# Performance work log

Measured on AMD Instinct MI355X. Metric: run time of the kernel, lower is better.

## Reference

```python
import jax, jax.numpy as jnp
import numpy as np

NEG_INF = -9e9  # matches torch code's -9000000000.0


def setup_inputs() -> dict:
    key = jax.random.key(0)
    ks = jax.random.split(key, 12)
    B, N, L = 128, 32, 36
    Ds, Dv, H = 512, 1024, 512
    span_embeddings = jax.random.normal(ks[0], (B, N, Ds), dtype=jnp.float32)
    image_embeddings = jax.random.normal(ks[1], (B, L, Dv), dtype=jnp.float32)
    span_mask = jax.random.randint(ks[2], (B, N), 0, 2).astype(jnp.float32)
    image_mask = jax.random.randint(ks[3], (B, L), 0, 2).astype(jnp.float32)
    # BilinearPairWiseClassifier weight: maps span dim -> image dim
    Wg = jax.random.normal(ks[4], (Ds, Dv), dtype=jnp.float32) / np.sqrt(Ds)
    # SimplePairWiseClassifier MLP on concat(first, second, first*second)
    W1 = jax.random.normal(ks[5], (3 * Ds, H), dtype=jnp.float32) / np.sqrt(3 * Ds)
    b1 = jnp.zeros((H,), dtype=jnp.float32)
    W2 = jax.random.normal(ks[6], (H, H), dtype=jnp.float32) / np.sqrt(H)
    b2 = jnp.zeros((H,), dtype=jnp.float32)
    W3 = jax.random.normal(ks[7], (H, 1), dtype=jnp.float32) / np.sqrt(H)
    b3 = jnp.zeros((1,), dtype=jnp.float32)
    return {
        "span_embeddings": span_embeddings,
        "image_embeddings": image_embeddings,
        "span_mask": span_mask,
        "image_mask": image_mask,
        "Wg": Wg, "W1": W1, "b1": b1, "W2": W2, "b2": b2, "W3": W3, "b3": b3,
    }


def reference(span_embeddings, image_embeddings, span_mask, image_mask,
              Wg, W1, b1, W2, b2, W3, b3):
    B, N, Ds = span_embeddings.shape
    L = image_embeddings.shape[1]

    # ---- score_grounding (vectorized B^2 loop) ----
    # mention_scores[b] = bilinear(first[b], second[b]); the off-diagonal
    # 'score' in the original loop recomputes the SAME thing (only the mask
    # varies with jdx), so one (B,N,L) tensor suffices.
    M = jnp.einsum('bnd,de,ble->bnl', span_embeddings, Wg, image_embeddings)  # (B,N,L)
    # pairwise mask over doc pairs (i uses span_mask, j uses image_mask)
    pm = span_mask[:, None, :, None] * image_mask[None, :, None, :]  # (B,B,N,L)
    pm = jnp.where(pm != 0, pm, NEG_INF)
    w = jax.nn.softmax(pm.reshape(B, B, N * L), axis=-1).reshape(B, B, N, L)
    sent_scores = jnp.einsum('inl,ijnl->ij', M, w)  # (B,B)

    # ---- score_text: all span pairs via combinations(range(N), 2) ----
    iu, ju = np.triu_indices(N, k=1)  # same order as itertools.combinations
    first = span_embeddings[:, iu]    # (B,P,Ds)
    second = span_embeddings[:, ju]   # (B,P,Ds)
    feat = jnp.concatenate([first, second, first * second], axis=-1)  # (B,P,3Ds)
    h = jax.nn.relu(feat @ W1 + b1)
    h = jax.nn.relu(h @ W2 + b2)
    text_scores = (h @ W3 + b3)[..., 0]  # (B,P)

    # ---- contrastive loss over sentence-score matrix ----
    loss = (-jnp.sum(jax.nn.log_softmax(sent_scores, axis=1))
            - jnp.sum(jax.nn.log_softmax(sent_scores.T, axis=1))) / B
    return loss, M, text_scores
```

## Files before the change

### kernel.cpp

```cpp
#include <hip/hip_runtime.h>

#define B_  128
#define N_  32
#define L_  36
#define DS  512
#define DV  1024
#define H_  512
#define P_  496
#define R_  63488
#define LSE_BLKS 128

typedef __attribute__((ext_vector_type(8))) short bf16x8;
typedef __attribute__((ext_vector_type(4))) float f32x4;

__device__ __forceinline__ ushort f2bf(float x){
  unsigned u = __builtin_bit_cast(unsigned, x);
  return (ushort)((u + 0x7FFFu + ((u >> 16) & 1u)) >> 16);
}
__device__ __forceinline__ float bf2f(ushort u){
  unsigned v = ((unsigned)u) << 16;
  return __builtin_bit_cast(float, v);
}

__device__ __forceinline__ bf16x8 pkmul(bf16x8 a, bf16x8 b){
  bf16x8 o;
  #pragma unroll
  for (int e = 0; e < 8; ++e)
    o[e] = (short)f2bf(bf2f((ushort)a[e]) * bf2f((ushort)b[e]));
  return o;
}

__device__ __forceinline__ void gload16(const void* g, void* l){
  __builtin_amdgcn_global_load_lds((const __attribute__((address_space(1))) unsigned*)g,
                                   (__attribute__((address_space(3))) unsigned*)l, 16, 0, 0);
}

__device__ __forceinline__ float wave_sum(float v){
  #pragma unroll
  for (int m = 32; m >= 1; m >>= 1) v += __shfl_xor(v, m);
  return v;
}
__device__ __forceinline__ float wave_max(float v){
  #pragma unroll
  for (int m = 32; m >= 1; m >>= 1) v = fmaxf(v, __shfl_xor(v, m));
  return v;
}

#define SPAN_F4 524288
#define IMG_F4  1179648
#define CONV_BLKS ((SPAN_F4 + IMG_F4) / 256)
#define TR_BLKS   (512 * 5)
__global__ void prep_all(const float* __restrict__ span, const float* __restrict__ img,
                         const float* __restrict__ b3,
                         const float* __restrict__ Wg, const float* __restrict__ W1,
                         const float* __restrict__ W2,
                         const float* __restrict__ sm, const float* __restrict__ im,
                         ushort* __restrict__ spbf, ushort* __restrict__ imgbf,
                         float* __restrict__ text,
                         ushort* __restrict__ WgT, ushort* __restrict__ UVBT,
                         ushort* __restrict__ W1cT, ushort* __restrict__ W2T,
                         float* cnt_s, float* cnt_i, int* iu, int* ju, float* loss){
  __shared__ float tile[32][33];
  const int bid = blockIdx.x, tid = threadIdx.x;
  if (bid < CONV_BLKS){
    int idx = bid * 256 + tid;
    if (idx < R_) text[idx] = b3[0];
    const float* src; ushort* dst; int k;
    if (idx < SPAN_F4){ src = span; dst = spbf; k = idx; }
    else              { src = img;  dst = imgbf; k = idx - SPAN_F4; }
    float4 v = *(const float4*)&src[(size_t)k * 4];
    ushort4 o; o.x = f2bf(v.x); o.y = f2bf(v.y); o.z = f2bf(v.z); o.w = f2bf(v.w);
    *(ushort4*)&dst[(size_t)k * 4] = o;
  } else if (bid < CONV_BLKS + TR_BLKS){
    int b = bid - CONV_BLKS;
    int z = b >> 9, rem = b & 511;
    int bx = rem & 31, by = rem >> 5;
    const float* src; ushort* dst; int Nn;
    if      (z == 0){ src = Wg;            dst = WgT;            Nn = 1024; }
    else if (z == 1){ src = W1;            dst = UVBT;           Nn = 512;  }
    else if (z == 2){ src = W1 + 512*512;  dst = UVBT + 512*512; Nn = 512;  }
    else if (z == 3){ src = W1 + 1024*512; dst = W1cT;           Nn = 512;  }
    else            { src = W2;            dst = W2T;            Nn = 512;  }
    if (bx * 32 >= Nn) return;
    int n0 = bx * 32, k0 = by * 32;
    int x = tid & 31, y = tid >> 5;
    #pragma unroll
    for (int i = 0; i < 4; ++i) tile[y + 8*i][x] = src[(k0 + y + 8*i) * Nn + n0 + x];
    __syncthreads();
    #pragma unroll
    for (int i = 0; i < 4; ++i) dst[(n0 + y + 8*i) * 512 + k0 + x] = f2bf(tile[x][y + 8*i]);
  } else {
    int t = (bid - CONV_BLKS - TR_BLKS) * 256 + tid;
    if (t < P_){
      int i = 0, rem = t, cnt = N_ - 1;
      while (rem >= cnt){ rem -= cnt; ++i; --cnt; }
      iu[t] = i; ju[t] = i + 1 + rem;
    }
    if (t < B_){
      float s = 0.f;
      for (int n = 0; n < N_; ++n) s += sm[t*N_ + n];
      cnt_s[t] = s;
    } else if (t < 2*B_){
      int j = t - B_;
      float s = 0.f;
      for (int l = 0; l < L_; ++l) s += im[j*L_ + l];
      cnt_i[j] = s;
    }
    if (t == 0) loss[0] = 0.f;
  }
}

__device__ __forceinline__ void mfma_phase(const ushort* cA, const ushort* cB,
                                           int wm, int wn, int fm, int quad,
                                           f32x4 acc[4][4]){
  bf16x8 af[4], bg[4];
  #pragma unroll
  for (int i = 0; i < 4; ++i){
    af[i] = *(const bf16x8*)&cA[(wm + i * 16 + fm) * 32 + quad * 8];
    bg[i] = *(const bf16x8*)&cB[(wn + i * 16 + fm) * 32 + quad * 8];
  }
  asm volatile("s_waitcnt lgkmcnt(0)" ::: "memory");
  __builtin_amdgcn_s_barrier();
  #pragma unroll
  for (int i = 0; i < 4; ++i)
    #pragma unroll
    for (int j = 0; j < 4; ++j)
      acc[i][j] = __builtin_amdgcn_mfma_f32_16x16x32_bf16(af[i], bg[j], acc[i][j], 0, 0, 0);
}

__device__ __forceinline__ void mma_mainloop(const ushort* __restrict__ A,
                                             const ushort* __restrict__ BT,
                                             size_t m0, int n0,
                                             ushort* sA0, ushort* sA1,
                                             ushort* sB0, ushort* sB1,
                                             f32x4 acc[4][4]){
  const int tid = threadIdx.x, wid = tid >> 6, lane = tid & 63;
  const int wm = (wid >> 1) * 64, wn = (wid & 1) * 64;
  const int quad = lane >> 4, fm = lane & 15;
  const char* gA = (const char*)A + (m0 + (size_t)(wid * 32 + (lane >> 2))) * 1024 + (lane & 3) * 16;
  const char* gB = (const char*)BT + ((size_t)n0 + wid * 32 + (lane >> 2)) * 1024 + (lane & 3) * 16;
  const int wb = wid * 1024;

  #define STG_ML(dA, dB, ks)                                   \
    do {                                                       \
      gload16(gA + (ks) * 64,             (dA) + wb);          \
      gload16(gA + (ks) * 64 + 16 * 1024, (dA) + wb + 512);    \
      gload16(gB + (ks) * 64,             (dB) + wb);          \
      gload16(gB + (ks) * 64 + 16 * 1024, (dB) + wb + 512);    \
    } while (0)

  STG_ML(sA0, sB0, 0);
  #pragma unroll
  for (int ks = 0; ks < 16; ks += 2){
    STG_ML(sA1, sB1, ks + 1);
    asm volatile("s_waitcnt vmcnt(4)" ::: "memory");
    __builtin_amdgcn_s_barrier();
    mfma_phase(sA0, sB0, wm, wn, fm, quad, acc);
    if (ks + 2 < 16){
      STG_ML(sA0, sB0, ks + 2);
      asm volatile("s_waitcnt vmcnt(4)" ::: "memory");
    } else {
      asm volatile("s_waitcnt vmcnt(0)" ::: "memory");
    }
    __builtin_amdgcn_s_barrier();
    mfma_phase(sA1, sB1, wm, wn, fm, quad, acc);
  }
  #undef STG_ML
}

__global__ __launch_bounds__(256, 4) void span2_makez(const ushort* __restrict__ A,
                                                      const ushort* __restrict__ BT2,
                                                      ushort* __restrict__ SG,
                                                      ushort* __restrict__ UV,
                                                      const int* __restrict__ iu,
                                                      const int* __restrict__ ju,
                                                      ushort* __restrict__ Z){
  __shared__ ushort sA0[4096], sA1[4096], sB0[4096], sB1[4096];
  if (blockIdx.x < 512){
    f32x4 acc[4][4] = {};
    size_t m0 = (size_t)(blockIdx.x >> 4) * 128;
    int ng = (blockIdx.x & 15) * 128;
    mma_mainloop(A, BT2, m0, ng, sA0, sA1, sB0, sB1, acc);
    const int tid = threadIdx.x, wid = tid >> 6, lane = tid & 63;
    const int wm = (wid >> 1) * 64, wn = (wid & 1) * 64, quad = lane >> 4, fm = lane & 15;
    ushort* C = (ng < 1024) ? SG : UV;
    const int nbase = (ng < 1024) ? ng : (ng - 1024);
    #pragma unroll
    for (int i = 0; i < 4; ++i)
      #pragma unroll
      for (int r = 0; r < 4; ++r){
        size_t row = m0 + wm + i * 16 + quad * 4 + r;
        #pragma unroll
        for (int j = 0; j < 4; ++j){
          int col = nbase + wn + j * 16 + fm;
          C[row * 1024 + col] = f2bf(acc[i][j][r]);
        }
      }
  } else {
    int idx = (blockIdx.x - 512) * 256 + threadIdx.x;
    int r = idx >> 6, k = (idx & 63) << 3;
    int b = r / P_, p = r - b * P_;
    bf16x8 x = *(const bf16x8*)&A[(size_t)(b * N_ + iu[p]) * 512 + k];
    bf16x8 y = *(const bf16x8*)&A[(size_t)(b * N_ + ju[p]) * 512 + k];
    *(bf16x8*)&Z[(size_t)r * 512 + k] = pkmul(x, y);
  }
}

__global__ __launch_bounds__(256) void batched_m_mfma(const ushort* __restrict__ SGbf,
                                                      const ushort* __restrict__ imgbf,
                                                      const float* __restrict__ sm,
                                                      float* __restrict__ Mout,
                                                      float* __restrict__ Msum,
                                                      float* __restrict__ Mtot){
  const int b = blockIdx.x;
  const int tid = threadIdx.x, wid = tid >> 6, lane = tid & 63;
  const int quad = lane >> 4, fm = lane & 15;
  __shared__ float red[4][32][48];
  __shared__ float shr[4];
  f32x4 acc[2][3] = {};
  const int wk = wid * 256;
  const ushort* Ab = SGbf + (size_t)b * 32 * 1024;
  const ushort* Bb = imgbf + (size_t)b * 36 * 1024;
  #pragma unroll
  for (int ks = 0; ks < 8; ++ks){
    const int k = wk + ks * 32 + quad * 8;
    bf16x8 af[2], bg[3];
    af[0] = *(const bf16x8*)&Ab[(0*16 + fm) * 1024 + k];
    af[1] = *(const bf16x8*)&Ab[(1*16 + fm) * 1024 + k];
    bg[0] = *(const bf16x8*)&Bb[(0*16 + fm) * 1024 + k];
    bg[1] = *(const bf16x8*)&Bb[(1*16 + fm) * 1024 + k];
    bg[2] = *(const bf16x8*)&Bb[(2*16 + fm) * 1024 + k];
    #pragma unroll
    for (int i = 0; i < 2; ++i)
      #pragma unroll
      for (int j = 0; j < 3; ++j)
        acc[i][j] = __builtin_amdgcn_mfma_f32_16x16x32_bf16(af[i], bg[j], acc[i][j], 0, 0, 0);
  }
  #pragma unroll
  for (int i = 0; i < 2; ++i)
    #pragma unroll
    for (int j = 0; j < 3; ++j)
      #pragma unroll
      for (int r = 0; r < 4; ++r)
        red[wid][i*16 + quad*4 + r][j*16 + fm] = acc[i][j][r];
  __syncthreads();
  float tot = 0.f;
  #pragma unroll
  for (int q = 0; q < 5; ++q){
    int out = tid + 256 * q;
    if (out < N_*L_){
      int n = out / L_, l = out - n * L_;
      float v = red[0][n][l] + red[1][n][l] + red[2][n][l] + red[3][n][l];
      Mout[b * (N_*L_) + out] = v;
      tot += v;
    }
  }
  tot = wave_sum(tot);
  if (lane == 0) shr[wid] = tot;
  __syncthreads();
  if (tid == 0) Mtot[b] = shr[0] + shr[1] + shr[2] + shr[3];
  if (tid < L_){
    float s = 0.f;
    for (int n = 0; n < N_; ++n){
      float mv = red[0][n][tid] + red[1][n][tid] + red[2][n][tid] + red[3][n][tid];
      s += mv * sm[b*N_ + n];
    }
    Msum[b*L_ + tid] = s;
  }
}

__device__ void lse_loss_body(const float* __restrict__ Msum, const float* __restrict__ im,
                              const float* __restrict__ cnt_s, const float* __restrict__ cnt_i,
                              const float* __restrict__ Mtot, float* __restrict__ out,
                              int i, float* sh ){
  const int tid = threadIdx.x;
  const int t = tid & 127;
  const int w4 = tid >> 6, lane = tid & 63;
  float sr = 0.f, sc = 0.f;
  #pragma unroll 4
  for (int l = 0; l < L_; ++l){
    sr += Msum[i*L_ + l] * im[t*L_ + l];
    sc += Msum[t*L_ + l] * im[i*L_ + l];
  }
  const float dr = cnt_s[i] * cnt_i[t];
  const float vr = (dr != 0.f) ? (sr / dr) : (Mtot[i] * (1.f/(float)(N_*L_)));
  const float dc = cnt_s[t] * cnt_i[i];
  const float vc = (dc != 0.f) ? (sc / dc) : (Mtot[t] * (1.f/(float)(N_*L_)));

  float m = wave_max(vr);
  if (lane == 0) sh[w4] = m;
  __syncthreads();
  const float mr = fmaxf(sh[0], sh[1]);
  __syncthreads();
  float e = wave_sum(expf(vr - mr));
  if (lane == 0) sh[w4] = e;
  __syncthreads();
  const float ser = sh[0] + sh[1];
  __syncthreads();
  float rs = wave_sum(vr);
  if (lane == 0) sh[w4] = rs;
  __syncthreads();
  const float rst = sh[0] + sh[1];
  __syncthreads();
  float mc0 = wave_max(vc);
  if (lane == 0) sh[w4] = mc0;
  __syncthreads();
  const float mc = fmaxf(sh[0], sh[1]);
  __syncthreads();
  float ec = wave_sum(expf(vc - mc));
  if (lane == 0) sh[w4] = ec;
  __syncthreads();
  const float sec = sh[0] + sh[1];
  if (tid == 0){
    float contrib = (mr + logf(ser)) + (mc + logf(sec)) - 2.f * rst / (float)B_;
    atomicAdd(out, contrib);
  }
}

__device__ __forceinline__ void mma_loop_k64(const ushort* __restrict__ A,
                                             const ushort* __restrict__ BT,
                                             size_t m0, int n0,
                                             ushort* sA0, ushort* sA1,
                                             ushort* sB0, ushort* sB1,
                                             f32x4 acc[4][4]){
  const int tid = threadIdx.x, wid = tid >> 6, lane = tid & 63;
  const int wm = (wid >> 1) * 64, wn = (wid & 1) * 64;
  const int quad = lane >> 4, fm = lane & 15;
  const int r64 = tid >> 2, ch = (tid & 3) * 8;
  const ushort* gA = A + (m0 + r64) * 512 + ch;
  const ushort* gB = BT + (size_t)(n0 + r64) * 512 + ch;

  #define STG_K(dA, dB, ks)                                   \
    do {                                                      \
      const int k0_ = (ks) * 32;                              \
      gload16(gA + k0_,            (dA) + tid * 8);           \
      gload16(gA + 64*512 + k0_,   (dA) + 2048 + tid * 8);    \
      gload16(gB + k0_,            (dB) + tid * 8);           \
      gload16(gB + 64*512 + k0_,   (dB) + 2048 + tid * 8);    \
    } while (0)

  STG_K(sA0, sB0, 0);
  #pragma unroll
  for (int ks = 0; ks < 16; ks += 2){
    STG_K(sA1, sB1, ks + 1);
    asm volatile("s_waitcnt vmcnt(4)" ::: "memory");
    __builtin_amdgcn_s_barrier();
    mfma_phase(sA0, sB0, wm, wn, fm, quad, acc);
    if (ks + 2 < 16){
      STG_K(sA0, sB0, ks + 2);
      asm volatile("s_waitcnt vmcnt(4)" ::: "memory");
    } else {
      asm volatile("s_waitcnt vmcnt(0)" ::: "memory");
    }
    __builtin_amdgcn_s_barrier();
    mfma_phase(sA1, sB1, wm, wn, fm, quad, acc);
  }
  #undef STG_K
}

__device__ __forceinline__ void tile_map(int bid, int& m0, int& n0){
  int x = bid & 7;
  int q = bid >> 3;
  int m = x * 62 + (q >> 2);
  m0 = m * 128;
  n0 = (q & 3) * 128;
}

__global__ __launch_bounds__(256, 4) void gemm_z(const ushort* __restrict__ Z,
                                                 const ushort* __restrict__ W1cT,
                                                 const ushort* __restrict__ UV,
                                                 const float* __restrict__ b1,
                                                 const int* __restrict__ iu,
                                                 const int* __restrict__ ju,
                                                 ushort* __restrict__ h1){
  __shared__ ushort sA0[4096], sA1[4096], sB0[4096], sB1[4096];
  f32x4 acc[4][4] = {};
  int m0i, n0; tile_map(blockIdx.x, m0i, n0);
  const size_t m0 = (size_t)m0i;
  mma_loop_k64(Z, W1cT, m0, n0, sA0, sA1, sB0, sB1, acc);
  const int tid = threadIdx.x, wid = tid >> 6, lane = tid & 63;
  const int wm = (wid >> 1) * 64, wn = (wid & 1) * 64, quad = lane >> 4, fm = lane & 15;
  #pragma unroll
  for (int i = 0; i < 4; ++i)
    #pragma unroll
    for (int r = 0; r < 4; ++r){
      int row = (int)m0 + wm + i * 16 + quad * 4 + r;
      int b = row / P_, p = row - b * P_;
      const ushort* Ur = UV + (size_t)(b * N_ + iu[p]) * 1024;
      const ushort* Vr = UV + (size_t)(b * N_ + ju[p]) * 1024 + 512;
      #pragma unroll
      for (int j = 0; j < 4; ++j){
        int col = n0 + wn + j * 16 + fm;
        float h = acc[i][j][r] + bf2f(Ur[col]) + bf2f(Vr[col]) + b1[col];
        h1[(size_t)row * 512 + col] = f2bf(fmaxf(h, 0.f));
      }
    }
}

__global__ __launch_bounds__(256, 4) void gemm_h2(const ushort* __restrict__ h1,
                                                  const ushort* __restrict__ W2T,
                                                  const float* __restrict__ b2,
                                                  const float* __restrict__ W3,
                                                  float* __restrict__ text,
                                                  const float* __restrict__ Msum,
                                                  const float* __restrict__ im,
                                                  const float* __restrict__ cnt_s,
                                                  const float* __restrict__ cnt_i,
                                                  const float* __restrict__ Mtot,
                                                  float* __restrict__ loss){
  __shared__ ushort smem[16384];
  if (blockIdx.x < LSE_BLKS){
    lse_loss_body(Msum, im, cnt_s, cnt_i, Mtot, loss, blockIdx.x, (float*)smem);
    return;
  }
  ushort* sA0 = smem;
  ushort* sA1 = smem + 4096;
  ushort* sB0 = smem + 8192;
  ushort* sB1 = smem + 12288;
  f32x4 acc[4][4] = {};
  int m0i, n0; tile_map(blockIdx.x - LSE_BLKS, m0i, n0);
  const size_t m0 = (size_t)m0i;
  mma_loop_k64(h1, W2T, m0, n0, sA0, sA1, sB0, sB1, acc);
  const int tid = threadIdx.x, wid = tid >> 6, lane = tid & 63;
  const int wm = (wid >> 1) * 64, wn = (wid & 1) * 64, quad = lane >> 4, fm = lane & 15;
  float w3v[4], b2v[4];
  #pragma unroll
  for (int j = 0; j < 4; ++j){
    int col = n0 + wn + j * 16 + fm;
    w3v[j] = W3[col]; b2v[j] = b2[col];
  }
  #pragma unroll
  for (int i = 0; i < 4; ++i)
    #pragma unroll
    for (int r = 0; r < 4; ++r){
      int row = (int)m0 + wm + i * 16 + quad * 4 + r;
      float s = 0.f;
      #pragma unroll
      for (int j = 0; j < 4; ++j){
        float h = fmaxf(acc[i][j][r] + b2v[j], 0.f);
        s = fmaf(h, w3v[j], s);
      }
      s += __shfl_xor(s, 1); s += __shfl_xor(s, 2); s += __shfl_xor(s, 4); s += __shfl_xor(s, 8);
      if (fm == 0) atomicAdd(&text[row], s);
    }
}

extern "C" void kernel_launch(void* const* d_in, const int* in_sizes, int n_in,
                              void* d_out, int out_size, void* d_ws, size_t ws_size,
                              hipStream_t stream) {
  const float* span = (const float*)d_in[0];
  const float* img  = (const float*)d_in[1];
  const float* sm   = (const float*)d_in[2];
  const float* im   = (const float*)d_in[3];
  const float* Wg   = (const float*)d_in[4];
  const float* W1   = (const float*)d_in[5];
  const float* b1   = (const float*)d_in[6];
  const float* W2   = (const float*)d_in[7];
  const float* b2   = (const float*)d_in[8];
  const float* W3   = (const float*)d_in[9];
  const float* b3   = (const float*)d_in[10];

  float* out  = (float*)d_out;
  float* loss = out;
  float* Mout = out + 1;
  float* text = out + 1 + B_*N_*L_;

  ushort* wsu  = (ushort*)d_ws;
  ushort* Zbf  = wsu;
  ushort* h1bf = Zbf + (size_t)R_*512;
  ushort* UVbf = h1bf + (size_t)R_*512;
  ushort* SGbf = UVbf + (size_t)4096*1024;
  ushort* spbf = SGbf + (size_t)4096*1024;
  ushort* imgbf= spbf + 4096*512;
  ushort* BT2  = imgbf + (size_t)(B_*L_ + 12)*1024;
  ushort* WgT  = BT2;
  ushort* UVBT = BT2 + 1024*512;
  ushort* W1cT = UVBT + 1024*512;
  ushort* W2T  = W1cT + 512*512;
  float* Msum  = (float*)(W2T + 512*512);
  float* Mtot  = Msum + B_*L_;
  float* cnt_s = Mtot + B_;
  float* cnt_i = cnt_s + B_;
  int*   iu    = (int*)(cnt_i + B_);
  int*   ju    = iu + P_;

  prep_all<<<CONV_BLKS + TR_BLKS + 2, 256, 0, stream>>>(
      span, img, b3, Wg, W1, W2, sm, im,
      spbf, imgbf, text, WgT, UVBT, W1cT, W2T, cnt_s, cnt_i, iu, ju, loss);

  span2_makez<<<512 + R_*512/8/256, 256, 0, stream>>>(spbf, BT2, SGbf, UVbf, iu, ju, Zbf);

  batched_m_mfma<<<B_, 256, 0, stream>>>(SGbf, imgbf, sm, Mout, Msum, Mtot);

  gemm_z<<<1984, 256, 0, stream>>>(Zbf, W1cT, UVbf, b1, iu, ju, h1bf);
  gemm_h2<<<LSE_BLKS + 1984, 256, 0, stream>>>(
      h1bf, W2T, b2, W3, text, Msum, im, cnt_s, cnt_i, Mtot, loss);
}
```

Before: 237.1 us.

## Triple-buffer LDS staging in GEMM mainloops with MFMA priority boost

```diff
diff --git a/kernel.cpp b/kernel.cpp
--- a/kernel.cpp
+++ b/kernel.cpp
@@ -110,29 +110,30 @@
   }
 }
 
-__device__ __forceinline__ void mfma_phase(const ushort* cA, const ushort* cB,
-                                           int wm, int wn, int fm, int quad,
-                                           f32x4 acc[4][4]){
-  bf16x8 af[4], bg[4];
+__device__ __forceinline__ void frag_ld(const ushort* cA, const ushort* cB,
+                                        int wm, int wn, int fm, int quad,
+                                        bf16x8 af[4], bf16x8 bg[4]){
   #pragma unroll
   for (int i = 0; i < 4; ++i){
     af[i] = *(const bf16x8*)&cA[(wm + i * 16 + fm) * 32 + quad * 8];
     bg[i] = *(const bf16x8*)&cB[(wn + i * 16 + fm) * 32 + quad * 8];
   }
-  asm volatile("s_waitcnt lgkmcnt(0)" ::: "memory");
-  __builtin_amdgcn_s_barrier();
+}
+__device__ __forceinline__ void mfma16(const bf16x8 af[4], const bf16x8 bg[4], f32x4 acc[4][4]){
+  __builtin_amdgcn_s_setprio(1);
   #pragma unroll
   for (int i = 0; i < 4; ++i)
     #pragma unroll
     for (int j = 0; j < 4; ++j)
       acc[i][j] = __builtin_amdgcn_mfma_f32_16x16x32_bf16(af[i], bg[j], acc[i][j], 0, 0, 0);
+  __builtin_amdgcn_s_setprio(0);
 }
 
 __device__ __forceinline__ void mma_mainloop(const ushort* __restrict__ A,
                                              const ushort* __restrict__ BT,
                                              size_t m0, int n0,
-                                             ushort* sA0, ushort* sA1,
-                                             ushort* sB0, ushort* sB1,
+                                             ushort* sA0, ushort* sA1, ushort* sA2,
+                                             ushort* sB0, ushort* sB1, ushort* sB2,
                                              f32x4 acc[4][4]){
   const int tid = threadIdx.x, wid = tid >> 6, lane = tid & 63;
   const int wm = (wid >> 1) * 64, wn = (wid & 1) * 64;
@@ -140,47 +141,48 @@
   const char* gA = (const char*)A + (m0 + (size_t)(wid * 32 + (lane >> 2))) * 1024 + (lane & 3) * 16;
   const char* gB = (const char*)BT + ((size_t)n0 + wid * 32 + (lane >> 2)) * 1024 + (lane & 3) * 16;
   const int wb = wid * 1024;
-
-  #define STG_ML(dA, dB, ks)                                   \
-    do {                                                       \
-      gload16(gA + (ks) * 64,             (dA) + wb);          \
-      gload16(gA + (ks) * 64 + 16 * 1024, (dA) + wb + 512);    \
-      gload16(gB + (ks) * 64,             (dB) + wb);          \
-      gload16(gB + (ks) * 64 + 16 * 1024, (dB) + wb + 512);    \
+  ushort* const bA[3] = {sA0, sA1, sA2};
+  ushort* const bB[3] = {sB0, sB1, sB2};
+
+  #define STG_ML(bi, ks)                                           \
+    do {                                                           \
+      gload16(gA + (ks) * 64,             bA[bi] + wb);            \
+      gload16(gA + (ks) * 64 + 16 * 1024, bA[bi] + wb + 512);      \
+      gload16(gB + (ks) * 64,             bB[bi] + wb);            \
+      gload16(gB + (ks) * 64 + 16 * 1024, bB[bi] + wb + 512);      \
     } while (0)
 
-  STG_ML(sA0, sB0, 0);
-  #pragma unroll
-  for (int ks = 0; ks < 16; ks += 2){
-    STG_ML(sA1, sB1, ks + 1);
-    asm volatile("s_waitcnt vmcnt(4)" ::: "memory");
+  STG_ML(0, 0); STG_ML(1, 1); STG_ML(2, 2);
+  #pragma unroll
+  for (int ks = 0; ks < 16; ++ks){
+    if (ks < 14)       asm volatile("s_waitcnt vmcnt(8)" ::: "memory");
+    else if (ks == 14) asm volatile("s_waitcnt vmcnt(4)" ::: "memory");
+    else               asm volatile("s_waitcnt vmcnt(0)" ::: "memory");
     __builtin_amdgcn_s_barrier();
-    mfma_phase(sA0, sB0, wm, wn, fm, quad, acc);
-    if (ks + 2 < 16){
-      STG_ML(sA0, sB0, ks + 2);
-      asm volatile("s_waitcnt vmcnt(4)" ::: "memory");
-    } else {
-      asm volatile("s_waitcnt vmcnt(0)" ::: "memory");
-    }
+    bf16x8 af[4], bg[4];
+    frag_ld(bA[ks % 3], bB[ks % 3], wm, wn, fm, quad, af, bg);
+    asm volatile("s_waitcnt lgkmcnt(0)" ::: "memory");
+    __builtin_amdgcn_sched_barrier(0);
     __builtin_amdgcn_s_barrier();
-    mfma_phase(sA1, sB1, wm, wn, fm, quad, acc);
+    if (ks + 3 < 16) STG_ML(ks % 3, ks + 3);
+    mfma16(af, bg, acc);
   }
   #undef STG_ML
 }
 
-__global__ __launch_bounds__(256, 4) void span2_makez(const ushort* __restrict__ A,
+__global__ __launch_bounds__(256, 3) void span2_makez(const ushort* __restrict__ A,
                                                       const ushort* __restrict__ BT2,
                                                       ushort* __restrict__ SG,
                                                       ushort* __restrict__ UV,
                                                       const int* __restrict__ iu,
                                                       const int* __restrict__ ju,
                                                       ushort* __restrict__ Z){
-  __shared__ ushort sA0[4096], sA1[4096], sB0[4096], sB1[4096];
+  __shared__ ushort sA0[4096], sA1[4096], sA2[4096], sB0[4096], sB1[4096], sB2[4096];
   if (blockIdx.x < 512){
     f32x4 acc[4][4] = {};
     size_t m0 = (size_t)(blockIdx.x >> 4) * 128;
     int ng = (blockIdx.x & 15) * 128;
-    mma_mainloop(A, BT2, m0, ng, sA0, sA1, sB0, sB1, acc);
+    mma_mainloop(A, BT2, m0, ng, sA0, sA1, sA2, sB0, sB1, sB2, acc);
     const int tid = threadIdx.x, wid = tid >> 6, lane = tid & 63;
     const int wm = (wid >> 1) * 64, wn = (wid & 1) * 64, quad = lane >> 4, fm = lane & 15;
     ushort* C = (ng < 1024) ? SG : UV;
@@ -320,8 +322,8 @@
 __device__ __forceinline__ void mma_loop_k64(const ushort* __restrict__ A,
                                              const ushort* __restrict__ BT,
                                              size_t m0, int n0,
-                                             ushort* sA0, ushort* sA1,
-                                             ushort* sB0, ushort* sB1,
+                                             ushort* sA0, ushort* sA1, ushort* sA2,
+                                             ushort* sB0, ushort* sB1, ushort* sB2,
                                              f32x4 acc[4][4]){
   const int tid = threadIdx.x, wid = tid >> 6, lane = tid & 63;
   const int wm = (wid >> 1) * 64, wn = (wid & 1) * 64;
@@ -329,31 +331,32 @@
   const int r64 = tid >> 2, ch = (tid & 3) * 8;
   const ushort* gA = A + (m0 + r64) * 512 + ch;
   const ushort* gB = BT + (size_t)(n0 + r64) * 512 + ch;
-
-  #define STG_K(dA, dB, ks)                                   \
-    do {                                                      \
-      const int k0_ = (ks) * 32;                              \
-      gload16(gA + k0_,            (dA) + tid * 8);           \
-      gload16(gA + 64*512 + k0_,   (dA) + 2048 + tid * 8);    \
-      gload16(gB + k0_,            (dB) + tid * 8);           \
-      gload16(gB + 64*512 + k0_,   (dB) + 2048 + tid * 8);    \
+  ushort* const bA[3] = {sA0, sA1, sA2};
+  ushort* const bB[3] = {sB0, sB1, sB2};
+
+  #define STG_K(bi, ks)                                        \
+    do {                                                       \
+      const int k0_ = (ks) * 32;                               \
+      gload16(gA + k0_,            bA[bi] + tid * 8);          \
+      gload16(gA + 64*512 + k0_,   bA[bi] + 2048 + tid * 8);   \
+      gload16(gB + k0_,            bB[bi] + tid * 8);          \
+      gload16(gB + 64*512 + k0_,   bB[bi] + 2048 + tid * 8);   \
     } while (0)
 
-  STG_K(sA0, sB0, 0);
-  #pragma unroll
-  for (int ks = 0; ks < 16; ks += 2){
-    STG_K(sA1, sB1, ks + 1);
-    asm volatile("s_waitcnt vmcnt(4)" ::: "memory");
+  STG_K(0, 0); STG_K(1, 1); STG_K(2, 2);
+  #pragma unroll
+  for (int ks = 0; ks < 16; ++ks){
+    if (ks < 14)       asm volatile("s_waitcnt vmcnt(8)" ::: "memory");
+    else if (ks == 14) asm volatile("s_waitcnt vmcnt(4)" ::: "memory");
+    else               asm volatile("s_waitcnt vmcnt(0)" ::: "memory");
     __builtin_amdgcn_s_barrier();
-    mfma_phase(sA0, sB0, wm, wn, fm, quad, acc);
-    if (ks + 2 < 16){
-      STG_K(sA0, sB0, ks + 2);
-      asm volatile("s_waitcnt vmcnt(4)" ::: "memory");
-    } else {
-      asm volatile("s_waitcnt vmcnt(0)" ::: "memory");
-    }
+    bf16x8 af[4], bg[4];
+    frag_ld(bA[ks % 3], bB[ks % 3], wm, wn, fm, quad, af, bg);
+    asm volatile("s_waitcnt lgkmcnt(0)" ::: "memory");
+    __builtin_amdgcn_sched_barrier(0);
     __builtin_amdgcn_s_barrier();
-    mfma_phase(sA1, sB1, wm, wn, fm, quad, acc);
+    if (ks + 3 < 16) STG_K(ks % 3, ks + 3);
+    mfma16(af, bg, acc);
   }
   #undef STG_K
 }
@@ -366,18 +369,18 @@
   n0 = (q & 3) * 128;
 }
 
-__global__ __launch_bounds__(256, 4) void gemm_z(const ushort* __restrict__ Z,
+__global__ __launch_bounds__(256, 3) void gemm_z(const ushort* __restrict__ Z,
                                                  const ushort* __restrict__ W1cT,
                                                  const ushort* __restrict__ UV,
                                                  const float* __restrict__ b1,
                                                  const int* __restrict__ iu,
                                                  const int* __restrict__ ju,
                                                  ushort* __restrict__ h1){
-  __shared__ ushort sA0[4096], sA1[4096], sB0[4096], sB1[4096];
+  __shared__ ushort sA0[4096], sA1[4096], sA2[4096], sB0[4096], sB1[4096], sB2[4096];
   f32x4 acc[4][4] = {};
   int m0i, n0; tile_map(blockIdx.x, m0i, n0);
   const size_t m0 = (size_t)m0i;
-  mma_loop_k64(Z, W1cT, m0, n0, sA0, sA1, sB0, sB1, acc);
+  mma_loop_k64(Z, W1cT, m0, n0, sA0, sA1, sA2, sB0, sB1, sB2, acc);
   const int tid = threadIdx.x, wid = tid >> 6, lane = tid & 63;
   const int wm = (wid >> 1) * 64, wn = (wid & 1) * 64, quad = lane >> 4, fm = lane & 15;
   #pragma unroll
@@ -397,7 +400,7 @@
     }
 }
 
-__global__ __launch_bounds__(256, 4) void gemm_h2(const ushort* __restrict__ h1,
+__global__ __launch_bounds__(256, 3) void gemm_h2(const ushort* __restrict__ h1,
                                                   const ushort* __restrict__ W2T,
                                                   const float* __restrict__ b2,
                                                   const float* __restrict__ W3,
@@ -408,19 +411,21 @@
                                                   const float* __restrict__ cnt_i,
                                                   const float* __restrict__ Mtot,
                                                   float* __restrict__ loss){
-  __shared__ ushort smem[16384];
+  __shared__ ushort smem[24576];
   if (blockIdx.x < LSE_BLKS){
     lse_loss_body(Msum, im, cnt_s, cnt_i, Mtot, loss, blockIdx.x, (float*)smem);
     return;
   }
   ushort* sA0 = smem;
   ushort* sA1 = smem + 4096;
-  ushort* sB0 = smem + 8192;
-  ushort* sB1 = smem + 12288;
+  ushort* sA2 = smem + 8192;
+  ushort* sB0 = smem + 12288;
+  ushort* sB1 = smem + 16384;
+  ushort* sB2 = smem + 20480;
   f32x4 acc[4][4] = {};
   int m0i, n0; tile_map(blockIdx.x - LSE_BLKS, m0i, n0);
   const size_t m0 = (size_t)m0i;
-  mma_loop_k64(h1, W2T, m0, n0, sA0, sA1, sB0, sB1, acc);
+  mma_loop_k64(h1, W2T, m0, n0, sA0, sA1, sA2, sB0, sB1, sB2, acc);
   const int tid = threadIdx.x, wid = tid >> 6, lane = tid & 63;
   const int wm = (wid >> 1) * 64, wn = (wid & 1) * 64, quad = lane >> 4, fm = lane & 15;
   float w3v[4], b2v[4];
```

New measurement: 244.8 us. +3.2%, slower.
